# Optimization experiments

Measured on AMD Instinct MI355X. Metric: run time of the kernel, lower is better.

Reference implementation:

```python
import jax, jax.numpy as jnp
import numpy as np
import math

D_MODEL = 512
N_HEADS = 8
D_FF = 2048
TOP_FACTOR = 5
LN_EPS = 1e-5


def _layernorm(x, g, b):
    m = jnp.mean(x, axis=-1, keepdims=True)
    v = jnp.mean((x - m) ** 2, axis=-1, keepdims=True)
    return (x - m) / jnp.sqrt(v + LN_EPS) * g + b


def _prob_sparse_attn(q_in, k_in, v_in, wq, bq, wk, bk, wv, bv, wo, bo):
    # weights stored (in, out): y = x @ w + b  (equivalent to torch Linear)
    B, Lq, dm = q_in.shape
    Lk = k_in.shape[1]
    H, D = N_HEADS, dm // N_HEADS
    q = (q_in @ wq + bq).reshape(B, Lq, H, D).transpose(0, 2, 1, 3)  # (B,H,Lq,D)
    k = (k_in @ wk + bk).reshape(B, Lk, H, D).transpose(0, 2, 1, 3)
    v = (v_in @ wv + bv).reshape(B, Lk, H, D).transpose(0, 2, 1, 3)

    qn = q / jnp.linalg.norm(q, axis=-1, keepdims=True)
    kn = k / jnp.linalg.norm(k, axis=-1, keepdims=True)
    # full cosine-similarity matrix, reduced to a row mean (as in the original)
    scores_all = jnp.einsum('bhqd,bhkd->bhqk', qn, kn)
    mean_scores = scores_all.mean(axis=-1)  # (B,H,Lq)

    u = max(1, Lq // TOP_FACTOR)
    _, top_idx = jax.lax.top_k(mean_scores, u)  # (B,H,u)

    q_sel = jnp.take_along_axis(q, top_idx[..., None], axis=2)  # (B,H,u,D)
    scores = jnp.einsum('bhud,bhkd->bhuk', q_sel, k) / math.sqrt(D)
    attn = jax.nn.softmax(scores, axis=-1)
    ctx_sel = jnp.einsum('bhuk,bhkd->bhud', attn, v)  # (B,H,u,D)

    b_ix = jnp.arange(B)[:, None, None]
    h_ix = jnp.arange(H)[None, :, None]
    context = jnp.zeros((B, H, Lq, D), dtype=q.dtype).at[b_ix, h_ix, top_idx].set(ctx_sel)
    out = context.transpose(0, 2, 1, 3).reshape(B, Lq, dm)
    return out @ wo + bo


def _decoder_layer(x, enc_out, p):
    xn = _layernorm(x, p['ln1_g'], p['ln1_b'])
    x = x + _prob_sparse_attn(xn, xn, xn, p['sa_wq'], p['sa_bq'], p['sa_wk'], p['sa_bk'],
                              p['sa_wv'], p['sa_bv'], p['sa_wo'], p['sa_bo'])
    xn = _layernorm(x, p['ln2_g'], p['ln2_b'])
    x = x + _prob_sparse_attn(xn, enc_out, enc_out, p['ca_wq'], p['ca_bq'], p['ca_wk'], p['ca_bk'],
                              p['ca_wv'], p['ca_bv'], p['ca_wo'], p['ca_bo'])
    xn = _layernorm(x, p['ln3_g'], p['ln3_b'])
    h = jax.nn.relu(xn @ p['ff_w1'] + p['ff_b1'])
    return x + (h @ p['ff_w2'] + p['ff_b2'])


def setup_inputs() -> dict:
    key = jax.random.key(0)
    ks = iter(jax.random.split(key, 32))
    B, L = 2, 2048
    dm, dff = D_MODEL, D_FF
    s = 1.0 / math.sqrt(dm)
    inp = {
        'x': jax.random.normal(next(ks), (B, L, dm), jnp.float32),
        'enc_out': jax.random.normal(next(ks), (B, L, dm), jnp.float32),
    }
    for pre in ('sa', 'ca'):
        for nm in ('wq', 'wk', 'wv', 'wo'):
            inp[f'{pre}_{nm}'] = jax.random.normal(next(ks), (dm, dm), jnp.float32) * s
            inp[f'{pre}_{nm[1:] and "b" + nm[1:]}'] = jnp.zeros((dm,), jnp.float32)
    inp['ff_w1'] = jax.random.normal(next(ks), (dm, dff), jnp.float32) * s
    inp['ff_b1'] = jnp.zeros((dff,), jnp.float32)
    inp['ff_w2'] = jax.random.normal(next(ks), (dff, dm), jnp.float32) / math.sqrt(dff)
    inp['ff_b2'] = jnp.zeros((dm,), jnp.float32)
    for i in (1, 2, 3):
        inp[f'ln{i}_g'] = jnp.ones((dm,), jnp.float32)
        inp[f'ln{i}_b'] = jnp.zeros((dm,), jnp.float32)
    return inp


def reference(x, enc_out,
              sa_wq, sa_bq, sa_wk, sa_bk, sa_wv, sa_bv, sa_wo, sa_bo,
              ca_wq, ca_bq, ca_wk, ca_bk, ca_wv, ca_bv, ca_wo, ca_bo,
              ff_w1, ff_b1, ff_w2, ff_b2,
              ln1_g, ln1_b, ln2_g, ln2_b, ln3_g, ln3_b):
    p = dict(sa_wq=sa_wq, sa_bq=sa_bq, sa_wk=sa_wk, sa_bk=sa_bk, sa_wv=sa_wv, sa_bv=sa_bv,
             sa_wo=sa_wo, sa_bo=sa_bo, ca_wq=ca_wq, ca_bq=ca_bq, ca_wk=ca_wk, ca_bk=ca_bk,
             ca_wv=ca_wv, ca_bv=ca_bv, ca_wo=ca_wo, ca_bo=ca_bo,
             ff_w1=ff_w1, ff_b1=ff_b1, ff_w2=ff_w2, ff_b2=ff_b2,
             ln1_g=ln1_g, ln1_b=ln1_b, ln2_g=ln2_g, ln2_b=ln2_b, ln3_g=ln3_g, ln3_b=ln3_b)
    return _decoder_layer(x, enc_out, p)
```

## Files before the change

kernel.cpp:

```cpp
#include <hip/hip_runtime.h>

#define BB 2
#define LL 2048
#define DM 512
#define NH 8
#define DH 64
#define DFF 2048
#define UU 409
#define ROWS (BB*LL)
#define X_ELEMS 2097152
#define IN_TOTAL 8398336
#define NCHUNK 16

typedef unsigned short u16;
typedef __attribute__((ext_vector_type(8))) short short8;
typedef __attribute__((ext_vector_type(4))) float floatx4;

#define G_TOTAL 38900000
__device__ float g_buf[G_TOTAL];
__device__ int   g_isbf16;

#define A_XN    8398336
#define A_Q     10495488
#define A_K     12592640
#define A_V     14689792
#define A_CTX   16786944
#define A_ENC   18884096
#define A_H     20981248
#define A_MKN   23078400
#define A_MS    23079424
#define A_SEL   23112192
#define A_PARTK 23144960
#define A_LIST  23177728
#define A_PART2 23184384
#define A_WT    30426112
#define XN_H    16796672
#define XN_L    18893824
#define CTX_H   33573888
#define CTX_L   35671040
#define ENC_H   37768192
#define ENC_L   39865344
#define AH_H    41962496
#define WT_SAQKV 60852224
#define WT_SAO   62425088
#define WT_CAQ   62949376
#define WT_CAKV  63473664
#define WT_CAO   64522240
#define WT_W1    65046528
#define WT_W2    67143680
#define KH_U    69240832
#define KL_U    71337984
#define VTH_U   73435136
#define VTL_U   75532288

__constant__ int c_end[28] = {
    2097152, 4194304, 4456448, 4456960, 4719104, 4719616, 4981760, 4982272,
    5244416, 5244928, 5507072, 5507584, 5769728, 5770240, 6032384, 6032896,
    6295040, 6295552, 7344128, 7346176, 8394752, 8395264, 8395776, 8396288,
    8396800, 8397312, 8397824, 8398336
};

__device__ __forceinline__ float bf2f(u16 x) {
    union { unsigned int u; float f; } c; c.u = ((unsigned int)x) << 16; return c.f;
}
__device__ __forceinline__ u16 f2bf(float f) {
    union { float f; unsigned int u; } c; c.f = f;
    unsigned int u = c.u;
    return (u16)((u + 0x7FFFu + ((u >> 16) & 1u)) >> 16);
}

struct P28 { const void* p[28]; };
struct I3 { int v[3]; };
__global__ void cvt_all(P28 ps) {
    const int f = (((const u16*)ps.p[22])[0] == 0x3F80u) ? 1 : 0;
    if (blockIdx.x == 0 && threadIdx.x == 0) g_isbf16 = f;
    int stride = gridDim.x * blockDim.x;
    u16* gb16 = (u16*)g_buf;
    for (int idx = blockIdx.x * blockDim.x + threadIdx.x; idx < IN_TOTAL; idx += stride) {
        int s = 0;
        while (idx >= c_end[s]) s++;
        int start = (s == 0) ? 0 : c_end[s - 1];
        int local = idx - start;
        float v;
        if (f) v = bf2f(((const u16*)ps.p[s])[local]);
        else   v = ((const float*)ps.p[s])[local];
        g_buf[idx] = v;
        if (s == 1) {
            u16 hi = f2bf(v);
            gb16[ENC_H + local] = hi;
            gb16[ENC_L + local] = f2bf(v - bf2f(hi));
        }
    }
}

__constant__ int tj[10][6] = {
    {4194304, WT_SAQKV, 0,    512,  786432, 8},
    {4456960, WT_SAQKV, 512,  512,  786432, 8},
    {4719616, WT_SAQKV, 1024, 512,  786432, 8},
    {4982272, WT_SAO,   0,    512,  262144, 8},
    {5244928, WT_CAQ,   0,    512,  262144, 8},
    {5507584, WT_CAKV,  0,    512,  524288, 8},
    {5770240, WT_CAKV,  512,  512,  524288, 8},
    {6032896, WT_CAO,   0,    512,  262144, 8},
    {6295552, WT_W1,    0,    512, 1048576, 32},
    {7346176, WT_W2,    0,   2048, 1048576, 8},
};
__constant__ int tcum[10] = {64, 128, 192, 256, 320, 384, 448, 512, 768, 1024};
__global__ void transpose_all() {
    int bid = blockIdx.x;
    int j = 0;
    while (bid >= tcum[j]) j++;
    int t = bid - (j ? tcum[j - 1] : 0);
    int w_off = tj[j][0], wt = tj[j][1], col0 = tj[j][2];
    int K = tj[j][3], lo = tj[j][4], txn = tj[j][5];
    int Nsrc = txn * 64;
    int n0 = (t % txn) * 64, k0 = (t / txn) * 64;
    __shared__ float tb[64][65];
    int c = threadIdx.x & 63, r0 = threadIdx.x >> 6;
    const float* W = g_buf + w_off;
    u16* WTh = ((u16*)g_buf) + wt;
    for (int i = 0; i < 16; i++) {
        int r = r0 + 4 * i;
        tb[r][c] = W[(size_t)(k0 + r) * Nsrc + n0 + c];
    }
    __syncthreads();
    for (int i = 0; i < 16; i++) {
        int r = r0 + 4 * i;
        float v = tb[c][r];
        u16 hi = f2bf(v);
        size_t o = (size_t)(col0 + n0 + r) * K + k0 + c;
        WTh[o] = hi;
        WTh[lo + o] = f2bf(v - bf2f(hi));
    }
}

__global__ void lnorm_k(int x_off, int g_off, int b_off, int yh_u16, int yl_u16) {
    int row = blockIdx.x;
    int tid = threadIdx.x;
    const float* x = g_buf + x_off + (size_t)row * DM;
    float a = x[tid], c = x[tid + 256];
    float s1 = a + c, s2 = a * a + c * c;
    for (int o = 32; o > 0; o >>= 1) { s1 += __shfl_xor(s1, o); s2 += __shfl_xor(s2, o); }
    __shared__ float r1[4], r2[4];
    int wave = tid >> 6, lane = tid & 63;
    if (lane == 0) { r1[wave] = s1; r2[wave] = s2; }
    __syncthreads();
    s1 = r1[0] + r1[1] + r1[2] + r1[3];
    s2 = r2[0] + r2[1] + r2[2] + r2[3];
    float mean = s1 * (1.0f / DM);
    float var  = s2 * (1.0f / DM) - mean * mean;
    float rstd = rsqrtf(var + 1e-5f);
    const float* gg = g_buf + g_off;
    const float* bb = g_buf + b_off;
    u16* yh = ((u16*)g_buf) + yh_u16 + (size_t)row * DM;
    u16* yl = ((u16*)g_buf) + yl_u16 + (size_t)row * DM;
    float v1 = (a - mean) * rstd * gg[tid]       + bb[tid];
    float v2 = (c - mean) * rstd * gg[tid + 256] + bb[tid + 256];
    u16 h1 = f2bf(v1), h2 = f2bf(v2);
    yh[tid] = h1;       yl[tid] = f2bf(v1 - bf2f(h1));
    yh[tid + 256] = h2; yl[tid + 256] = f2bf(v2 - bf2f(h2));
}

template<int WM, bool SPLIT, bool SEC, bool RELU, bool RESID, bool FINAL, bool OUTH>
__global__ void mgemm_k(int a_u16, int wt_u16_off, I3 boffs, int resid_off,
                        int out_off, void* __restrict__ dext, int M, int N, int K) {
    constexpr int BT_M = WM * 32;
    constexpr int A4 = BT_M * 4;
    __shared__ u16 Ash[BT_M * 40];
    __shared__ u16 Asl[SPLIT ? BT_M * 40 : 8];
    __shared__ u16 Bsh[128 * 40];
    __shared__ u16 Bsl[SPLIT ? 128 * 40 : 8];
    const u16* Ah = ((const u16*)g_buf) + a_u16;
    const u16* Al = Ah + (size_t)M * K;
    const u16* WTh = ((const u16*)g_buf) + wt_u16_off;
    const u16* WTl = WTh + (size_t)N * K;
    int isbf = FINAL ? g_isbf16 : 0;
    int tid = threadIdx.x;
    int lane = tid & 63, wid = tid >> 6;
    int wm = wid >> 1, wn = wid & 1;
    int quad = lane >> 4, l15 = lane & 15;
    int m0 = blockIdx.y * BT_M, n0 = blockIdx.x * 128;
    floatx4 acc[WM][4];
#pragma unroll
    for (int i = 0; i < WM; i++)
#pragma unroll
        for (int j = 0; j < 4; j++) acc[i][j] = (floatx4){0.f, 0.f, 0.f, 0.f};
    for (int k0 = 0; k0 < K; k0 += 32) {
#pragma unroll
        for (int i = 0; i < (A4 + 255) / 256; i++) {
            int idx8 = tid + 256 * i;
            if (A4 % 256 == 0 || idx8 < A4) {
                int r = idx8 >> 2, c8 = (idx8 & 3) * 8;
                *(uint4*)(&Ash[r * 40 + c8]) = *(const uint4*)(Ah + (size_t)(m0 + r) * K + k0 + c8);
                if constexpr (SPLIT)
                    *(uint4*)(&Asl[r * 40 + c8]) = *(const uint4*)(Al + (size_t)(m0 + r) * K + k0 + c8);
            }
        }
#pragma unroll
        for (int i = 0; i < 2; i++) {
            int idx8 = tid + 256 * i;
            int r = idx8 >> 2, c8 = (idx8 & 3) * 8;
            *(uint4*)(&Bsh[r * 40 + c8]) = *(const uint4*)(WTh + (size_t)(n0 + r) * K + k0 + c8);
            if constexpr (SPLIT)
                *(uint4*)(&Bsl[r * 40 + c8]) = *(const uint4*)(WTl + (size_t)(n0 + r) * K + k0 + c8);
        }
        __syncthreads();
        short8 ah[WM], bh[4], al[WM], bl[4];
#pragma unroll
        for (int i = 0; i < WM; i++) {
            int ro = (wm * WM * 16 + i * 16 + l15) * 40 + quad * 8;
            ah[i] = *(const short8*)(&Ash[ro]);
            if constexpr (SPLIT) al[i] = *(const short8*)(&Asl[ro]);
        }
#pragma unroll
        for (int j = 0; j < 4; j++) {
            int ro = (wn * 64 + j * 16 + l15) * 40 + quad * 8;
            bh[j] = *(const short8*)(&Bsh[ro]);
            if constexpr (SPLIT) bl[j] = *(const short8*)(&Bsl[ro]);
        }
#pragma unroll
        for (int i = 0; i < WM; i++)
#pragma unroll
            for (int j = 0; j < 4; j++) {
                acc[i][j] = __builtin_amdgcn_mfma_f32_16x16x32_bf16(ah[i], bh[j], acc[i][j], 0, 0, 0);
                if constexpr (SPLIT) {
                    acc[i][j] = __builtin_amdgcn_mfma_f32_16x16x32_bf16(ah[i], bl[j], acc[i][j], 0, 0, 0);
                    acc[i][j] = __builtin_amdgcn_mfma_f32_16x16x32_bf16(al[i], bh[j], acc[i][j], 0, 0, 0);
                }
            }
        __syncthreads();
    }
#pragma unroll
    for (int i = 0; i < WM; i++)
#pragma unroll
        for (int j = 0; j < 4; j++)
#pragma unroll
            for (int r = 0; r < 4; r++) {
                int row = m0 + wm * WM * 16 + i * 16 + quad * 4 + r;
                int col = n0 + wn * 64 + j * 16 + l15;
                int sec = SEC ? (col >> 9) : 0;
                int ci  = SEC ? (col & 511) : col;
                float v = acc[i][j][r] + g_buf[boffs.v[sec] + ci];
                if (RELU) v = fmaxf(v, 0.f);
                if (RESID) v += g_buf[resid_off + (size_t)row * N + col];
                if (FINAL) {
                    if (isbf) ((u16*)dext)[(size_t)row * N + col] = f2bf(v);
                    else      ((float*)dext)[(size_t)row * N + col] = v;
                } else if (OUTH) {
                    ((u16*)g_buf)[out_off + (size_t)row * N + col] = f2bf(v);
                } else if (SEC) {
                    g_buf[out_off + ((size_t)sec * M + row) * 512 + ci] = v;
                } else {
                    g_buf[out_off + (size_t)row * N + col] = v;
                }
            }
}

__global__ void prep_attn(int k_off, int v_off) {
    int kb = blockIdx.x, bh = blockIdx.y;
    int b = bh >> 3, h = bh & 7;
    int tid = threadIdx.x;
    int tok = tid >> 2, c = (tid & 3) * 16;
    u16* KH = (u16*)g_buf + KH_U + (size_t)bh * LL * 64;
    u16* KL = (u16*)g_buf + KL_U + (size_t)bh * LL * 64;
    u16* VTH = (u16*)g_buf + VTH_U + (size_t)bh * 64 * LL;
    u16* VTL = (u16*)g_buf + VTL_U + (size_t)bh * 64 * LL;
    {
        const float* kp = g_buf + k_off + ((size_t)(b * LL + kb * 64 + tok)) * DM + h * DH + c;
        float v[16] __attribute__((aligned(16)));
#pragma unroll
        for (int i = 0; i < 4; i++) *(float4*)(v + 4 * i) = *(const float4*)(kp + 4 * i);
        u16 hh[16] __attribute__((aligned(16)));
        u16 lo[16] __attribute__((aligned(16)));
#pragma unroll
        for (int i = 0; i < 16; i++) { u16 hi = f2bf(v[i]); hh[i] = hi; lo[i] = f2bf(v[i] - bf2f(hi)); }
        size_t o = (size_t)(kb * 64 + tok) * 64 + c;
        *(uint4*)(&KH[o]) = ((const uint4*)hh)[0]; *(uint4*)(&KH[o + 8]) = ((const uint4*)hh)[1];
        *(uint4*)(&KL[o]) = ((const uint4*)lo)[0]; *(uint4*)(&KL[o + 8]) = ((const uint4*)lo)[1];
    }
    __shared__ float vt[64][65];
    {
        const float* vp = g_buf + v_off + ((size_t)(b * LL + kb * 64 + tok)) * DM + h * DH + c;
#pragma unroll
        for (int i = 0; i < 16; i++) vt[tok][c + i] = vp[i];
    }
    __syncthreads();
    {
        int d = tid >> 2, ck = (tid & 3) * 16;
        u16 hh[16] __attribute__((aligned(16)));
        u16 lo[16] __attribute__((aligned(16)));
#pragma unroll
        for (int i = 0; i < 16; i++) {
            float x = vt[ck + i][d];
            u16 hi = f2bf(x); hh[i] = hi; lo[i] = f2bf(x - bf2f(hi));
        }
        size_t o = (size_t)d * LL + kb * 64 + ck;
        *(uint4*)(&VTH[o]) = ((const uint4*)hh)[0]; *(uint4*)(&VTH[o + 8]) = ((const uint4*)hh)[1];
        *(uint4*)(&VTL[o]) = ((const uint4*)lo)[0]; *(uint4*)(&VTL[o + 8]) = ((const uint4*)lo)[1];
    }
}

__global__ void meankn_p1(int k_off, int part_off) {
    int bh = blockIdx.x >> 5, chunk = blockIdx.x & 31;
    int b = bh >> 3, h = bh & 7;
    int wave = threadIdx.x >> 6, lane = threadIdx.x & 63;
    const float* base = g_buf + k_off + (size_t)b * LL * DM + (size_t)h * DH + lane;
    float acc = 0.f;
    for (int t = 0; t < 16; t++) {
        int j = chunk * 64 + wave * 16 + t;
        float kv = base[(size_t)j * DM];
        float s = kv * kv;
        for (int o = 32; o > 0; o >>= 1) s += __shfl_xor(s, o);
        acc += kv / sqrtf(fmaxf(s, 1e-30f));
    }
    __shared__ float red[4][64];
    red[wave][lane] = acc;
    __syncthreads();
    if (threadIdx.x < 64)
        g_buf[part_off + (size_t)blockIdx.x * 64 + threadIdx.x] =
            red[0][threadIdx.x] + red[1][threadIdx.x] + red[2][threadIdx.x] + red[3][threadIdx.x];
}
__global__ void meankn_p2(int part_off, int mkn_off) {
    int bh = blockIdx.x; int lane = threadIdx.x;
    float s = 0.f;
    for (int c = 0; c < 32; c++) s += g_buf[part_off + (size_t)(bh * 32 + c) * 64 + lane];
    g_buf[mkn_off + bh * 64 + lane] = s * (1.0f / LL);
}

__global__ void mscore_k(int q_off, int mkn_off, int ms_off) {
    int row = blockIdx.x * 4 + (threadIdx.x >> 6);
    int lane = threadIdx.x & 63;
    int q = row & (LL - 1);
    int bh = row >> 11;
    int b = bh >> 3, h = bh & 7;
    float qv = g_buf[q_off + ((size_t)b * LL + q) * DM + h * DH + lane];
    float m = g_buf[mkn_off + bh * 64 + lane];
    float s = qv * qv, d = qv * m;
    for (int o = 32; o > 0; o >>= 1) { s += __shfl_xor(s, o); d += __shfl_xor(d, o); }
    if (lane == 0) g_buf[ms_off + row] = d / sqrtf(fmaxf(s, 1e-30f));
}

__global__ void topsel_k(int ms_off, int sel_off, int u) {
    __shared__ float s[LL];
    int bh = blockIdx.y, chunk = blockIdx.x;
    for (int i = threadIdx.x; i < LL; i += 256) s[i] = g_buf[ms_off + bh * LL + i];
    __syncthreads();
    int il = threadIdx.x >> 2;
    int i = chunk * 64 + il;
    int jq = threadIdx.x & 3;
    float si = s[i];
    int cnt = 0;
    for (int t = 0; t < 512; t++) {
        int j = jq * 512 + t;
        float sj = s[j];
        cnt += (sj > si) || (sj == si && j < i);
    }
    cnt += __shfl_xor(cnt, 1);
    cnt += __shfl_xor(cnt, 2);
    if (jq == 0) ((int*)(g_buf + sel_off))[bh * LL + i] = (cnt < u) ? 1 : 0;
}

__global__ void compact_k(int sel_off, int list_off) {
    __shared__ int cnts[256];
    __shared__ int pref[256];
    int bh = blockIdx.x, tid = threadIdx.x;
    const int* sel = (const int*)(g_buf + sel_off) + bh * LL;
    int* list = (int*)(g_buf + list_off) + bh * 416;
    int c = 0;
    for (int j = 0; j < 8; j++) c += sel[tid * 8 + j];
    cnts[tid] = c;
    __syncthreads();
    if (tid == 0) { int run = 0; for (int i = 0; i < 256; i++) { pref[i] = run; run += cnts[i]; } }
    __syncthreads();
    int base = pref[tid];
    for (int j = 0; j < 8; j++) {
        int i = tid * 8 + j;
        if (sel[i]) list[base++] = i;
    }
}

__global__ void zero_k(int off, int n) {
    int i = blockIdx.x * blockDim.x + threadIdx.x;
    int st = gridDim.x * blockDim.x;
    for (; i < n; i += st) g_buf[off + i] = 0.f;
}

__global__ void attn_flash(int q_off, int list_off, int part_off, int u) {
    int bh = blockIdx.y, b = bh >> 3, h = bh & 7;
    int chunk = blockIdx.z;
    int tid = threadIdx.x, lane = tid & 63, w = tid >> 6;
    int quad = lane >> 4, l15 = lane & 15;
    const int* list = (const int*)(g_buf + list_off);

    short8 qh[2][2], ql[2][2];
#pragma unroll
    for (int g = 0; g < 2; g++) {
        int slot_q = blockIdx.x * 128 + w * 32 + g * 16 + l15;
        int qidx = list[bh * 416 + (slot_q < u ? slot_q : u - 1)];
        const float* qp = g_buf + q_off + ((size_t)b * LL + qidx) * DM + h * DH;
#pragma unroll
        for (int d2 = 0; d2 < 2; d2++) {
            float v[8] __attribute__((aligned(16)));
            *(float4*)(v)     = *(const float4*)(qp + d2 * 32 + quad * 8);
            *(float4*)(v + 4) = *(const float4*)(qp + d2 * 32 + quad * 8 + 4);
            u16 hh[8] __attribute__((aligned(16)));
            u16 lo[8] __attribute__((aligned(16)));
#pragma unroll
            for (int j = 0; j < 8; j++) {
                float s = v[j] * 0.125f;
                u16 hi = f2bf(s); hh[j] = hi; lo[j] = f2bf(s - bf2f(hi));
            }
            qh[g][d2] = *(const short8*)hh; ql[g][d2] = *(const short8*)lo;
        }
    }

    __shared__ u16 Ksh[64 * 68], Ksl[64 * 68];
    __shared__ u16 Vth[64 * 68], Vtl[64 * 68];
    __shared__ float Ps[4][16 * 68];

    float m_run[2][4], l_run[2][4];
    floatx4 acc_o[2][4];
#pragma unroll
    for (int g = 0; g < 2; g++)
#pragma unroll
        for (int r = 0; r < 4; r++) { m_run[g][r] = -3.0e38f; l_run[g][r] = 0.f; }
#pragma unroll
    for (int g = 0; g < 2; g++)
#pragma unroll
        for (int j = 0; j < 4; j++) acc_o[g][j] = (floatx4){0.f, 0.f, 0.f, 0.f};

    const u16* KHp = (const u16*)g_buf + KH_U + (size_t)bh * LL * 64;
    const u16* KLp = (const u16*)g_buf + KL_U + (size_t)bh * LL * 64;
    const u16* VTHp = (const u16*)g_buf + VTH_U + (size_t)bh * 64 * LL;
    const u16* VTLp = (const u16*)g_buf + VTL_U + (size_t)bh * 64 * LL;

    for (int kt = 0; kt < 2; kt++) {
        int row0 = chunk * 128 + kt * 64;
        {
            int r = tid >> 2, c = (tid & 3) * 16;
            const u16* s1 = KHp + (size_t)(row0 + r) * 64 + c;
            const u16* s2 = KLp + (size_t)(row0 + r) * 64 + c;
            *(uint4*)(&Ksh[r * 68 + c])     = *(const uint4*)(s1);
            *(uint4*)(&Ksh[r * 68 + c + 8]) = *(const uint4*)(s1 + 8);
            *(uint4*)(&Ksl[r * 68 + c])     = *(const uint4*)(s2);
            *(uint4*)(&Ksl[r * 68 + c + 8]) = *(const uint4*)(s2 + 8);
            const u16* s3 = VTHp + (size_t)r * LL + row0 + c;
            const u16* s4 = VTLp + (size_t)r * LL + row0 + c;
            *(uint4*)(&Vth[r * 68 + c])     = *(const uint4*)(s3);
            *(uint4*)(&Vth[r * 68 + c + 8]) = *(const uint4*)(s3 + 8);
            *(uint4*)(&Vtl[r * 68 + c])     = *(const uint4*)(s4);
            *(uint4*)(&Vtl[r * 68 + c + 8]) = *(const uint4*)(s4 + 8);
        }
        __syncthreads();
#pragma unroll
        for (int g = 0; g < 2; g++) {
            floatx4 sacc[4];
#pragma unroll
            for (int t = 0; t < 4; t++) {
                sacc[t] = (floatx4){0.f, 0.f, 0.f, 0.f};
#pragma unroll
                for (int d2 = 0; d2 < 2; d2++) {
                    int ro = (t * 16 + l15) * 68 + d2 * 32 + quad * 8;
                    short8 kh = *(const short8*)(&Ksh[ro]);
                    short8 kl = *(const short8*)(&Ksl[ro]);
                    sacc[t] = __builtin_amdgcn_mfma_f32_16x16x32_bf16(qh[g][d2], kh, sacc[t], 0, 0, 0);
                    sacc[t] = __builtin_amdgcn_mfma_f32_16x16x32_bf16(qh[g][d2], kl, sacc[t], 0, 0, 0);
                    sacc[t] = __builtin_amdgcn_mfma_f32_16x16x32_bf16(ql[g][d2], kh, sacc[t], 0, 0, 0);
                }
            }
            float alpha[4];
#pragma unroll
            for (int r = 0; r < 4; r++) {
                float mx = fmaxf(fmaxf(sacc[0][r], sacc[1][r]), fmaxf(sacc[2][r], sacc[3][r]));
                for (int o = 1; o < 16; o <<= 1) mx = fmaxf(mx, __shfl_xor(mx, o));
                float mn = fmaxf(m_run[g][r], mx);
                alpha[r] = __expf(m_run[g][r] - mn);
                m_run[g][r] = mn;
                float ls = 0.f;
#pragma unroll
                for (int t = 0; t < 4; t++) {
                    float p = __expf(sacc[t][r] - mn);
                    sacc[t][r] = p;
                    ls += p;
                }
                for (int o = 1; o < 16; o <<= 1) ls += __shfl_xor(ls, o);
                l_run[g][r] = l_run[g][r] * alpha[r] + ls;
            }
#pragma unroll
            for (int t = 0; t < 4; t++)
#pragma unroll
                for (int r = 0; r < 4; r++)
                    Ps[w][(quad * 4 + r) * 68 + t * 16 + l15] = sacc[t][r];
#pragma unroll
            for (int j = 0; j < 4; j++)
#pragma unroll
                for (int r = 0; r < 4; r++) acc_o[g][j][r] *= alpha[r];
#pragma unroll
            for (int s2 = 0; s2 < 2; s2++) {
                float pv[8] __attribute__((aligned(16)));
                *(float4*)(pv)     = *(const float4*)(&Ps[w][l15 * 68 + s2 * 32 + quad * 8]);
                *(float4*)(pv + 4) = *(const float4*)(&Ps[w][l15 * 68 + s2 * 32 + quad * 8 + 4]);
                u16 ph[8] __attribute__((aligned(16)));
                u16 pl[8] __attribute__((aligned(16)));
#pragma unroll
                for (int j = 0; j < 8; j++) { u16 hi = f2bf(pv[j]); ph[j] = hi; pl[j] = f2bf(pv[j] - bf2f(hi)); }
                short8 phv = *(const short8*)ph, plv = *(const short8*)pl;
#pragma unroll
                for (int j = 0; j < 4; j++) {
                    int ro = (j * 16 + l15) * 68 + s2 * 32 + quad * 8;
                    short8 vh = *(const short8*)(&Vth[ro]);
                    short8 vl = *(const short8*)(&Vtl[ro]);
                    acc_o[g][j] = __builtin_amdgcn_mfma_f32_16x16x32_bf16(phv, vh, acc_o[g][j], 0, 0, 0);
                    acc_o[g][j] = __builtin_amdgcn_mfma_f32_16x16x32_bf16(phv, vl, acc_o[g][j], 0, 0, 0);
                    acc_o[g][j] = __builtin_amdgcn_mfma_f32_16x16x32_bf16(plv, vh, acc_o[g][j], 0, 0, 0);
                }
            }
        }
        __syncthreads();
    }
#pragma unroll
    for (int g = 0; g < 2; g++)
#pragma unroll
        for (int r = 0; r < 4; r++) {
            int slot = blockIdx.x * 128 + w * 32 + g * 16 + quad * 4 + r;
            if (slot >= u) continue;
            float* pp = g_buf + part_off + (((size_t)bh * 416 + slot) * NCHUNK + chunk) * 68;
#pragma unroll
            for (int j = 0; j < 4; j++) pp[j * 16 + l15] = acc_o[g][j][r];
            if (l15 == 0) { pp[64] = m_run[g][r]; pp[65] = l_run[g][r]; }
        }
}

__global__ void attn_combine(int part_off, int list_off, int u) {
    int bh = blockIdx.y;
    int b = bh >> 3, h = bh & 7;
    int tid = threadIdx.x;
    int qi = tid >> 4;
    int kb = tid & 15;
    int ds = kb * 4;
    int slot = blockIdx.x * 16 + qi;
    if (slot >= u) return;
    int qidx = ((const int*)(g_buf + list_off))[bh * 416 + slot];
    const float* pp = g_buf + part_off + ((size_t)bh * 416 + slot) * NCHUNK * 68;
    float m = -3.0e38f;
#pragma unroll
    for (int c = 0; c < NCHUNK; c++) m = fmaxf(m, pp[c * 68 + 64]);
    float l = 0.f, O0 = 0.f, O1 = 0.f, O2 = 0.f, O3 = 0.f;
#pragma unroll
    for (int c = 0; c < NCHUNK; c++) {
        float a = __expf(pp[c * 68 + 64] - m);
        l += a * pp[c * 68 + 65];
        float4 o = *(const float4*)(pp + c * 68 + ds);
        O0 += a * o.x; O1 += a * o.y; O2 += a * o.z; O3 += a * o.w;
    }
    float inv = 1.0f / l;
    float o0 = O0 * inv, o1 = O1 * inv, o2 = O2 * inv, o3 = O3 * inv;
    size_t idx = ((size_t)b * LL + qidx) * DM + h * DH + ds;
    ushort4 hv, lv;
    hv.x = f2bf(o0); lv.x = f2bf(o0 - bf2f(hv.x));
    hv.y = f2bf(o1); lv.y = f2bf(o1 - bf2f(hv.y));
    hv.z = f2bf(o2); lv.z = f2bf(o2 - bf2f(hv.z));
    hv.w = f2bf(o3); lv.w = f2bf(o3 - bf2f(hv.w));
    *(ushort4*)(((u16*)g_buf) + CTX_H + idx) = hv;
    *(ushort4*)(((u16*)g_buf) + CTX_L + idx) = lv;
}

extern "C" void kernel_launch(void* const* d_in, const int* in_sizes, int n_in,
                              void* d_out, int out_size, void* d_ws, size_t ws_size,
                              hipStream_t stream) {
    static const int SZ[28] = {
        2097152, 2097152,
        262144, 512, 262144, 512, 262144, 512, 262144, 512,
        262144, 512, 262144, 512, 262144, 512, 262144, 512,
        1048576, 2048, 1048576, 512,
        512, 512, 512, 512, 512, 512
    };
    int OFF[28];
    int cur = 0;
    for (int i = 0; i < 28; i++) { OFF[i] = cur; cur += SZ[i]; }
    const int X = X_ELEMS;

    P28 ps;
    for (int i = 0; i < 28; i++) ps.p[i] = d_in[i];
    cvt_all<<<4096, 256, 0, stream>>>(ps);
    transpose_all<<<1024, 256, 0, stream>>>();

    auto select_attend = [&](void) {
        prep_attn<<<dim3(32, 16), 256, 0, stream>>>(A_K, A_V);
        meankn_p1<<<16 * 32, 256, 0, stream>>>(A_K, A_PARTK);
        meankn_p2<<<16, 64, 0, stream>>>(A_PARTK, A_MKN);
        mscore_k<<<(BB * NH * LL) / 4, 256, 0, stream>>>(A_Q, A_MKN, A_MS);
        topsel_k<<<dim3(32, 16), 256, 0, stream>>>(A_MS, A_SEL, UU);
        compact_k<<<BB * NH, 256, 0, stream>>>(A_SEL, A_LIST);
        zero_k<<<1024, 256, 0, stream>>>(A_CTX, X);
        attn_flash<<<dim3(4, 16, NCHUNK), 256, 0, stream>>>(A_Q, A_LIST, A_PART2, UU);
        attn_combine<<<dim3(26, 16), 256, 0, stream>>>(A_PART2, A_LIST, UU);
    };

    lnorm_k<<<ROWS, 256, 0, stream>>>(OFF[0], OFF[22], OFF[23], XN_H, XN_L);
    mgemm_k<2, true, true, false, false, false, false><<<dim3(12, 64), 256, 0, stream>>>(
        XN_H, WT_SAQKV, I3{{OFF[3], OFF[5], OFF[7]}}, 0, A_Q, nullptr, ROWS, 1536, 512);
    select_attend();
    mgemm_k<1, true, false, false, true, false, false><<<dim3(4, 128), 256, 0, stream>>>(
        CTX_H, WT_SAO, I3{{OFF[9], 0, 0}}, OFF[0], OFF[0], nullptr, ROWS, 512, 512);

    lnorm_k<<<ROWS, 256, 0, stream>>>(OFF[0], OFF[24], OFF[25], XN_H, XN_L);
    mgemm_k<1, true, false, false, false, false, false><<<dim3(4, 128), 256, 0, stream>>>(
        XN_H, WT_CAQ, I3{{OFF[11], 0, 0}}, 0, A_Q, nullptr, ROWS, 512, 512);
    mgemm_k<2, true, true, false, false, false, false><<<dim3(8, 64), 256, 0, stream>>>(
        ENC_H, WT_CAKV, I3{{OFF[13], OFF[15], 0}}, 0, A_K, nullptr, ROWS, 1024, 512);
    select_attend();
    mgemm_k<1, false, false, false, true, false, false><<<dim3(4, 128), 256, 0, stream>>>(
        CTX_H, WT_CAO, I3{{OFF[17], 0, 0}}, OFF[0], OFF[0], nullptr, ROWS, 512, 512);

    lnorm_k<<<ROWS, 256, 0, stream>>>(OFF[0], OFF[26], OFF[27], XN_H, XN_L);
    mgemm_k<4, false, false, true, false, false, true><<<dim3(16, 32), 256, 0, stream>>>(
        XN_H, WT_W1, I3{{OFF[19], 0, 0}}, 0, AH_H, nullptr, ROWS, 2048, 512);
    mgemm_k<1, false, false, false, true, true, false><<<dim3(4, 128), 256, 0, stream>>>(
        AH_H, WT_W2, I3{{OFF[21], 0, 0}}, OFF[0], 0, d_out, ROWS, 512, 2048);
}
```

Measured before the change: 652.4 us.

## Fuse K/V hi-lo split into attention kernel and widen query tiles per block

Drops the separate prep_attn pass and has attn_flash load fp32 K/V directly, split them into bf16 hi/lo and transpose V in shared memory. Each block now handles 256 query slots instead of 128, so K/V tiles are reused across more queries. Partial outputs move to a separate O and m/l layout, the cross-attention K/V GEMM is split into two GEMMs, and cvt_all uses a binary search for segment lookup. The cost is redundant conversion work repeated by each block and higher register pressure from the larger per-thread accumulators.

```diff
diff --git a/kernel.cpp b/kernel.cpp
--- a/kernel.cpp
+++ b/kernel.cpp
@@ -16,24 +16,21 @@
 typedef __attribute__((ext_vector_type(8))) short short8;
 typedef __attribute__((ext_vector_type(4))) float floatx4;
 
-#define G_TOTAL 38900000
+#define G_TOTAL 38200000
 __device__ float g_buf[G_TOTAL];
 __device__ int   g_isbf16;
 
-#define A_XN    8398336
 #define A_Q     10495488
 #define A_K     12592640
 #define A_V     14689792
-#define A_CTX   16786944
-#define A_ENC   18884096
-#define A_H     20981248
-#define A_MKN   23078400
-#define A_MS    23079424
-#define A_SEL   23112192
-#define A_PARTK 23144960
-#define A_LIST  23177728
-#define A_PART2 23184384
-#define A_WT    30426112
+#define A_MKN   25175552
+#define A_MS    25176576
+#define A_SEL   25209344
+#define A_PARTK 25242112
+#define A_LIST  25274880
+#define A_PO    25281536
+#define A_PML   33670144
+#define A_CTXF  16786944
 #define XN_H    16796672
 #define XN_L    18893824
 #define CTX_H   33573888
@@ -41,17 +38,14 @@
 #define ENC_H   37768192
 #define ENC_L   39865344
 #define AH_H    41962496
-#define WT_SAQKV 60852224
-#define WT_SAO   62425088
-#define WT_CAQ   62949376
-#define WT_CAKV  63473664
-#define WT_CAO   64522240
-#define WT_W1    65046528
-#define WT_W2    67143680
-#define KH_U    69240832
-#define KL_U    71337984
-#define VTH_U   73435136
-#define VTL_U   75532288
+#define WT_SAQKV 67864576
+#define WT_SAO   69437440
+#define WT_CAQ   69961728
+#define WT_CAK   70486016
+#define WT_CAV   71010304
+#define WT_CAO   71534592
+#define WT_W1    72058880
+#define WT_W2    74156032
 
 __constant__ int c_end[28] = {
     2097152, 4194304, 4456448, 4456960, 4719104, 4719616, 4981760, 4982272,
@@ -78,7 +72,11 @@
     u16* gb16 = (u16*)g_buf;
     for (int idx = blockIdx.x * blockDim.x + threadIdx.x; idx < IN_TOTAL; idx += stride) {
         int s = 0;
-        while (idx >= c_end[s]) s++;
+#pragma unroll
+        for (int step = 16; step >= 1; step >>= 1) {
+            int ns = s + step;
+            if (ns <= 27 && idx >= c_end[ns - 1]) s = ns;
+        }
         int start = (s == 0) ? 0 : c_end[s - 1];
         int local = idx - start;
         float v;
@@ -99,8 +97,8 @@
     {4719616, WT_SAQKV, 1024, 512,  786432, 8},
     {4982272, WT_SAO,   0,    512,  262144, 8},
     {5244928, WT_CAQ,   0,    512,  262144, 8},
-    {5507584, WT_CAKV,  0,    512,  524288, 8},
-    {5770240, WT_CAKV,  512,  512,  524288, 8},
+    {5507584, WT_CAK,   0,    512,  262144, 8},
+    {5770240, WT_CAV,   0,    512,  262144, 8},
     {6032896, WT_CAO,   0,    512,  262144, 8},
     {6295552, WT_W1,    0,    512, 1048576, 32},
     {7346176, WT_W2,    0,   2048, 1048576, 8},
@@ -249,55 +247,11 @@
                 } else if (OUTH) {
                     ((u16*)g_buf)[out_off + (size_t)row * N + col] = f2bf(v);
                 } else if (SEC) {
-                    g_buf[out_off + ((size_t)sec * M + row) * 512 + ci] = v;
+                    g_buf[out_off + ((size_t)sec * ROWS + row) * 512 + ci] = v;
                 } else {
                     g_buf[out_off + (size_t)row * N + col] = v;
                 }
             }
-}
-
-__global__ void prep_attn(int k_off, int v_off) {
-    int kb = blockIdx.x, bh = blockIdx.y;
-    int b = bh >> 3, h = bh & 7;
-    int tid = threadIdx.x;
-    int tok = tid >> 2, c = (tid & 3) * 16;
-    u16* KH = (u16*)g_buf + KH_U + (size_t)bh * LL * 64;
-    u16* KL = (u16*)g_buf + KL_U + (size_t)bh * LL * 64;
-    u16* VTH = (u16*)g_buf + VTH_U + (size_t)bh * 64 * LL;
-    u16* VTL = (u16*)g_buf + VTL_U + (size_t)bh * 64 * LL;
-    {
-        const float* kp = g_buf + k_off + ((size_t)(b * LL + kb * 64 + tok)) * DM + h * DH + c;
-        float v[16] __attribute__((aligned(16)));
-#pragma unroll
-        for (int i = 0; i < 4; i++) *(float4*)(v + 4 * i) = *(const float4*)(kp + 4 * i);
-        u16 hh[16] __attribute__((aligned(16)));
-        u16 lo[16] __attribute__((aligned(16)));
-#pragma unroll
-        for (int i = 0; i < 16; i++) { u16 hi = f2bf(v[i]); hh[i] = hi; lo[i] = f2bf(v[i] - bf2f(hi)); }
-        size_t o = (size_t)(kb * 64 + tok) * 64 + c;
-        *(uint4*)(&KH[o]) = ((const uint4*)hh)[0]; *(uint4*)(&KH[o + 8]) = ((const uint4*)hh)[1];
-        *(uint4*)(&KL[o]) = ((const uint4*)lo)[0]; *(uint4*)(&KL[o + 8]) = ((const uint4*)lo)[1];
-    }
-    __shared__ float vt[64][65];
-    {
-        const float* vp = g_buf + v_off + ((size_t)(b * LL + kb * 64 + tok)) * DM + h * DH + c;
-#pragma unroll
-        for (int i = 0; i < 16; i++) vt[tok][c + i] = vp[i];
-    }
-    __syncthreads();
-    {
-        int d = tid >> 2, ck = (tid & 3) * 16;
-        u16 hh[16] __attribute__((aligned(16)));
-        u16 lo[16] __attribute__((aligned(16)));
-#pragma unroll
-        for (int i = 0; i < 16; i++) {
-            float x = vt[ck + i][d];
-            u16 hi = f2bf(x); hh[i] = hi; lo[i] = f2bf(x - bf2f(hi));
-        }
-        size_t o = (size_t)d * LL + kb * 64 + ck;
-        *(uint4*)(&VTH[o]) = ((const uint4*)hh)[0]; *(uint4*)(&VTH[o + 8]) = ((const uint4*)hh)[1];
-        *(uint4*)(&VTL[o]) = ((const uint4*)lo)[0]; *(uint4*)(&VTL[o + 8]) = ((const uint4*)lo)[1];
-    }
 }
 
 __global__ void meankn_p1(int k_off, int part_off) {
@@ -385,17 +339,18 @@
     for (; i < n; i += st) g_buf[off + i] = 0.f;
 }
 
-__global__ void attn_flash(int q_off, int list_off, int part_off, int u) {
+__global__ __launch_bounds__(256, 2) void attn_flash(int q_off, int k_off, int v_off,
+        int list_off, int po_off, int pml_off, int u) {
     int bh = blockIdx.y, b = bh >> 3, h = bh & 7;
     int chunk = blockIdx.z;
     int tid = threadIdx.x, lane = tid & 63, w = tid >> 6;
     int quad = lane >> 4, l15 = lane & 15;
     const int* list = (const int*)(g_buf + list_off);
 
-    short8 qh[2][2], ql[2][2];
-#pragma unroll
-    for (int g = 0; g < 2; g++) {
-        int slot_q = blockIdx.x * 128 + w * 32 + g * 16 + l15;
+    short8 qh[4][2], ql[4][2];
+#pragma unroll
+    for (int g = 0; g < 4; g++) {
+        int slot_q = blockIdx.x * 256 + w * 64 + g * 16 + l15;
         int qidx = list[bh * 416 + (slot_q < u ? slot_q : u - 1)];
         const float* qp = g_buf + q_off + ((size_t)b * LL + qidx) * DM + h * DH;
 #pragma unroll
@@ -416,44 +371,59 @@
 
     __shared__ u16 Ksh[64 * 68], Ksl[64 * 68];
     __shared__ u16 Vth[64 * 68], Vtl[64 * 68];
-    __shared__ float Ps[4][16 * 68];
-
-    float m_run[2][4], l_run[2][4];
-    floatx4 acc_o[2][4];
-#pragma unroll
-    for (int g = 0; g < 2; g++)
-#pragma unroll
-        for (int r = 0; r < 4; r++) { m_run[g][r] = -3.0e38f; l_run[g][r] = 0.f; }
-#pragma unroll
-    for (int g = 0; g < 2; g++)
-#pragma unroll
-        for (int j = 0; j < 4; j++) acc_o[g][j] = (floatx4){0.f, 0.f, 0.f, 0.f};
-
-    const u16* KHp = (const u16*)g_buf + KH_U + (size_t)bh * LL * 64;
-    const u16* KLp = (const u16*)g_buf + KL_U + (size_t)bh * LL * 64;
-    const u16* VTHp = (const u16*)g_buf + VTH_U + (size_t)bh * 64 * LL;
-    const u16* VTLp = (const u16*)g_buf + VTL_U + (size_t)bh * 64 * LL;
+    __shared__ float smbuf[4352];
+
+    float m_run[4][4], l_run[4][4];
+    floatx4 acc_o[4][4];
+#pragma unroll
+    for (int g = 0; g < 4; g++)
+#pragma unroll
+        for (int r = 0; r < 4; r++) {
+            m_run[g][r] = -3.0e38f; l_run[g][r] = 0.f;
+            acc_o[g][r] = (floatx4){0.f, 0.f, 0.f, 0.f};
+        }
 
     for (int kt = 0; kt < 2; kt++) {
         int row0 = chunk * 128 + kt * 64;
+        __syncthreads();
         {
-            int r = tid >> 2, c = (tid & 3) * 16;
-            const u16* s1 = KHp + (size_t)(row0 + r) * 64 + c;
-            const u16* s2 = KLp + (size_t)(row0 + r) * 64 + c;
-            *(uint4*)(&Ksh[r * 68 + c])     = *(const uint4*)(s1);
-            *(uint4*)(&Ksh[r * 68 + c + 8]) = *(const uint4*)(s1 + 8);
-            *(uint4*)(&Ksl[r * 68 + c])     = *(const uint4*)(s2);
-            *(uint4*)(&Ksl[r * 68 + c + 8]) = *(const uint4*)(s2 + 8);
-            const u16* s3 = VTHp + (size_t)r * LL + row0 + c;
-            const u16* s4 = VTLp + (size_t)r * LL + row0 + c;
-            *(uint4*)(&Vth[r * 68 + c])     = *(const uint4*)(s3);
-            *(uint4*)(&Vth[r * 68 + c + 8]) = *(const uint4*)(s3 + 8);
-            *(uint4*)(&Vtl[r * 68 + c])     = *(const uint4*)(s4);
-            *(uint4*)(&Vtl[r * 68 + c + 8]) = *(const uint4*)(s4 + 8);
+            int tok = tid >> 2, c = (tid & 3) * 16;
+            const float* kp = g_buf + k_off + ((size_t)(b * LL + row0 + tok)) * DM + h * DH + c;
+            float v[16] __attribute__((aligned(16)));
+#pragma unroll
+            for (int i = 0; i < 4; i++) *(float4*)(v + 4 * i) = *(const float4*)(kp + 4 * i);
+            u16 hh[16] __attribute__((aligned(16)));
+            u16 lo[16] __attribute__((aligned(16)));
+#pragma unroll
+            for (int i = 0; i < 16; i++) { u16 hi = f2bf(v[i]); hh[i] = hi; lo[i] = f2bf(v[i] - bf2f(hi)); }
+            *(uint4*)(&Ksh[tok * 68 + c])     = ((const uint4*)hh)[0];
+            *(uint4*)(&Ksh[tok * 68 + c + 8]) = ((const uint4*)hh)[1];
+            *(uint4*)(&Ksl[tok * 68 + c])     = ((const uint4*)lo)[0];
+            *(uint4*)(&Ksl[tok * 68 + c + 8]) = ((const uint4*)lo)[1];
+            const float* vp = g_buf + v_off + ((size_t)(b * LL + row0 + tok)) * DM + h * DH + c;
+#pragma unroll
+            for (int i = 0; i < 4; i++)
+                *(float4*)(&smbuf[tok * 68 + c + 4 * i]) = *(const float4*)(vp + 4 * i);
         }
         __syncthreads();
-#pragma unroll
-        for (int g = 0; g < 2; g++) {
+        {
+            int d = tid >> 2, ck = (tid & 3) * 16;
+            u16 hh[16] __attribute__((aligned(16)));
+            u16 lo[16] __attribute__((aligned(16)));
+#pragma unroll
+            for (int i = 0; i < 16; i++) {
+                float x = smbuf[(ck + i) * 68 + d];
+                u16 hi = f2bf(x); hh[i] = hi; lo[i] = f2bf(x - bf2f(hi));
+            }
+            *(uint4*)(&Vth[d * 68 + ck])     = ((const uint4*)hh)[0];
+            *(uint4*)(&Vth[d * 68 + ck + 8]) = ((const uint4*)hh)[1];
+            *(uint4*)(&Vtl[d * 68 + ck])     = ((const uint4*)lo)[0];
+            *(uint4*)(&Vtl[d * 68 + ck + 8]) = ((const uint4*)lo)[1];
+        }
+        __syncthreads();
+        float* ps = smbuf + w * 1088;
+#pragma unroll
+        for (int g = 0; g < 4; g++) {
             floatx4 sacc[4];
 #pragma unroll
             for (int t = 0; t < 4; t++) {
@@ -490,7 +460,7 @@
             for (int t = 0; t < 4; t++)
 #pragma unroll
                 for (int r = 0; r < 4; r++)
-                    Ps[w][(quad * 4 + r) * 68 + t * 16 + l15] = sacc[t][r];
+                    ps[(quad * 4 + r) * 68 + t * 16 + l15] = sacc[t][r];
 #pragma unroll
             for (int j = 0; j < 4; j++)
 #pragma unroll
@@ -498,8 +468,8 @@
 #pragma unroll
             for (int s2 = 0; s2 < 2; s2++) {
                 float pv[8] __attribute__((aligned(16)));
-                *(float4*)(pv)     = *(const float4*)(&Ps[w][l15 * 68 + s2 * 32 + quad * 8]);
-                *(float4*)(pv + 4) = *(const float4*)(&Ps[w][l15 * 68 + s2 * 32 + quad * 8 + 4]);
+                *(float4*)(pv)     = *(const float4*)(&ps[l15 * 68 + s2 * 32 + quad * 8]);
+                *(float4*)(pv + 4) = *(const float4*)(&ps[l15 * 68 + s2 * 32 + quad * 8 + 4]);
                 u16 ph[8] __attribute__((aligned(16)));
                 u16 pl[8] __attribute__((aligned(16)));
 #pragma unroll
@@ -516,22 +486,25 @@
                 }
             }
         }
-        __syncthreads();
-    }
-#pragma unroll
-    for (int g = 0; g < 2; g++)
+    }
+#pragma unroll
+    for (int g = 0; g < 4; g++)
 #pragma unroll
         for (int r = 0; r < 4; r++) {
-            int slot = blockIdx.x * 128 + w * 32 + g * 16 + quad * 4 + r;
+            int slot = blockIdx.x * 256 + w * 64 + g * 16 + quad * 4 + r;
             if (slot >= u) continue;
-            float* pp = g_buf + part_off + (((size_t)bh * 416 + slot) * NCHUNK + chunk) * 68;
-#pragma unroll
-            for (int j = 0; j < 4; j++) pp[j * 16 + l15] = acc_o[g][j][r];
-            if (l15 == 0) { pp[64] = m_run[g][r]; pp[65] = l_run[g][r]; }
-        }
-}
-
-__global__ void attn_combine(int part_off, int list_off, int u) {
+            size_t rec = ((size_t)(bh * 16 + chunk)) * 512 + slot;
+            float* po = g_buf + po_off + rec * 64;
+#pragma unroll
+            for (int j = 0; j < 4; j++) po[j * 16 + l15] = acc_o[g][j][r];
+            if (l15 == 0) {
+                float* pml = g_buf + pml_off + rec * 2;
+                pml[0] = m_run[g][r]; pml[1] = l_run[g][r];
+            }
+        }
+}
+
+__global__ void attn_combine(int po_off, int pml_off, int list_off, int u) {
     int bh = blockIdx.y;
     int b = bh >> 3, h = bh & 7;
     int tid = threadIdx.x;
@@ -541,16 +514,18 @@
     int slot = blockIdx.x * 16 + qi;
     if (slot >= u) return;
     int qidx = ((const int*)(g_buf + list_off))[bh * 416 + slot];
-    const float* pp = g_buf + part_off + ((size_t)bh * 416 + slot) * NCHUNK * 68;
     float m = -3.0e38f;
 #pragma unroll
-    for (int c = 0; c < NCHUNK; c++) m = fmaxf(m, pp[c * 68 + 64]);
+    for (int c = 0; c < NCHUNK; c++)
+        m = fmaxf(m, g_buf[pml_off + (((size_t)(bh * 16 + c)) * 512 + slot) * 2]);
     float l = 0.f, O0 = 0.f, O1 = 0.f, O2 = 0.f, O3 = 0.f;
 #pragma unroll
     for (int c = 0; c < NCHUNK; c++) {
-        float a = __expf(pp[c * 68 + 64] - m);
-        l += a * pp[c * 68 + 65];
-        float4 o = *(const float4*)(pp + c * 68 + ds);
+        size_t rec = ((size_t)(bh * 16 + c)) * 512 + slot;
+        const float* pml = g_buf + pml_off + rec * 2;
+        float a = __expf(pml[0] - m);
+        l += a * pml[1];
+        float4 o = *(const float4*)(g_buf + po_off + rec * 64 + ds);
         O0 += a * o.x; O1 += a * o.y; O2 += a * o.z; O3 += a * o.w;
     }
     float inv = 1.0f / l;
@@ -578,7 +553,6 @@
     int OFF[28];
     int cur = 0;
     for (int i = 0; i < 28; i++) { OFF[i] = cur; cur += SZ[i]; }
-    const int X = X_ELEMS;
 
     P28 ps;
     for (int i = 0; i < 28; i++) ps.p[i] = d_in[i];
@@ -586,15 +560,14 @@
     transpose_all<<<1024, 256, 0, stream>>>();
 
     auto select_attend = [&](void) {
-        prep_attn<<<dim3(32, 16), 256, 0, stream>>>(A_K, A_V);
         meankn_p1<<<16 * 32, 256, 0, stream>>>(A_K, A_PARTK);
         meankn_p2<<<16, 64, 0, stream>>>(A_PARTK, A_MKN);
         mscore_k<<<(BB * NH * LL) / 4, 256, 0, stream>>>(A_Q, A_MKN, A_MS);
         topsel_k<<<dim3(32, 16), 256, 0, stream>>>(A_MS, A_SEL, UU);
         compact_k<<<BB * NH, 256, 0, stream>>>(A_SEL, A_LIST);
-        zero_k<<<1024, 256, 0, stream>>>(A_CTX, X);
-        attn_flash<<<dim3(4, 16, NCHUNK), 256, 0, stream>>>(A_Q, A_LIST, A_PART2, UU);
-        attn_combine<<<dim3(26, 16), 256, 0, stream>>>(A_PART2, A_LIST, UU);
+        zero_k<<<1024, 256, 0, stream>>>(A_CTXF, X_ELEMS);
+        attn_flash<<<dim3(2, 16, NCHUNK), 256, 0, stream>>>(A_Q, A_K, A_V, A_LIST, A_PO, A_PML, UU);
+        attn_combine<<<dim3(26, 16), 256, 0, stream>>>(A_PO, A_PML, A_LIST, UU);
     };
 
     lnorm_k<<<ROWS, 256, 0, stream>>>(OFF[0], OFF[22], OFF[23], XN_H, XN_L);
@@ -607,8 +580,10 @@
     lnorm_k<<<ROWS, 256, 0, stream>>>(OFF[0], OFF[24], OFF[25], XN_H, XN_L);
     mgemm_k<1, true, false, false, false, false, false><<<dim3(4, 128), 256, 0, stream>>>(
         XN_H, WT_CAQ, I3{{OFF[11], 0, 0}}, 0, A_Q, nullptr, ROWS, 512, 512);
-    mgemm_k<2, true, true, false, false, false, false><<<dim3(8, 64), 256, 0, stream>>>(
-        ENC_H, WT_CAKV, I3{{OFF[13], OFF[15], 0}}, 0, A_K, nullptr, ROWS, 1024, 512);
+    mgemm_k<1, true, false, false, false, false, false><<<dim3(4, 128), 256, 0, stream>>>(
+        ENC_H, WT_CAK, I3{{OFF[13], 0, 0}}, 0, A_K, nullptr, ROWS, 512, 512);
+    mgemm_k<1, false, false, false, false, false, false><<<dim3(4, 128), 256, 0, stream>>>(
+        ENC_H, WT_CAV, I3{{OFF[15], 0, 0}}, 0, A_V, nullptr, ROWS, 512, 512);
     select_attend();
     mgemm_k<1, false, false, false, true, false, false><<<dim3(4, 128), 256, 0, stream>>>(
         CTX_H, WT_CAO, I3{{OFF[17], 0, 0}}, OFF[0], OFF[0], nullptr, ROWS, 512, 512);
```

Result: faster. 603.9 us (-7.4%).
